# Optimization experiments

Measured on AMD Instinct MI355X. Metric: run time of the kernel, lower is better.

## Reference

```python
import jax, jax.numpy as jnp
import numpy as np

L, H, D, DFF, B, S = 4, 8, 512, 2048, 2, 2048
DH = D // H
EPS = 1e-5
SCALE_BASE = 512.0


def setup_inputs() -> dict:
    key = jax.random.key(0)
    ks = jax.random.split(key, 8)
    def w(k, shape, s=0.02):
        return jax.random.normal(k, shape, jnp.float32) * s
    return {
        "x": jax.random.normal(ks[0], (B, S, D), jnp.float32),
        "WQ": w(ks[1], (L, H, D, DH)),
        "WK": w(ks[2], (L, H, D, DH)),
        "WV": w(ks[3], (L, H, D, DH)),
        "WG": w(ks[4], (L, D, D)),
        "WO": w(ks[5], (L, D, D)),
        "gn_w": jnp.ones((L, D), jnp.float32),
        "gn_b": jnp.zeros((L, D), jnp.float32),
        "ln1_w": jnp.ones((L, D), jnp.float32),
        "ln1_b": jnp.zeros((L, D), jnp.float32),
        "ln2_w": jnp.ones((L, D), jnp.float32),
        "ln2_b": jnp.zeros((L, D), jnp.float32),
        "ffn_w1": w(ks[6], (L, D, DFF)),
        "ffn_b1": jnp.zeros((L, DFF), jnp.float32),
        "ffn_w2": w(ks[7], (L, DFF, D)),
        "ffn_b2": jnp.zeros((L, D), jnp.float32),
    }


def _dup(t):
    # duplicate_interleave: [a,b] -> [a,a,b,b]
    return jnp.repeat(t, 2, axis=-1)


def _rot(x):
    # rotate_every_two: (x1,x2) -> (-x2, x1)
    x1, x2 = x[..., ::2], x[..., 1::2]
    return jnp.stack([-x2, x1], axis=-1).reshape(x.shape)


def _xpos(x, downscale):
    # x: [B,H,S,dh]  XPOS rotary with length-extrapolating scale
    s_len, dh = x.shape[-2], x.shape[-1]
    half = dh // 2
    base = (jnp.arange(0, dh, 2, dtype=jnp.float32) + 0.4 * dh) / (1.4 * dh)  # [half]
    power = jnp.arange(s_len, dtype=jnp.float32) / SCALE_BASE
    scale = base[None, :] ** power[:, None]  # [S, half]
    if downscale:
        scale = 1.0 / scale
    inv_freq = 1.0 / (10000.0 ** (jnp.arange(half, dtype=jnp.float32) / half))
    ang = jnp.arange(s_len, dtype=jnp.float32)[:, None] * inv_freq[None, :]
    sin, cos, sc = _dup(jnp.sin(ang)), _dup(jnp.cos(ang)), _dup(scale)
    return x * cos * sc + _rot(x) * sin * sc


def _ln(x, w, b):
    mu = jnp.mean(x, -1, keepdims=True)
    var = jnp.mean((x - mu) ** 2, -1, keepdims=True)
    return (x - mu) * jax.lax.rsqrt(var + EPS) * w + b


def reference(x, WQ, WK, WV, WG, WO, gn_w, gn_b, ln1_w, ln1_b, ln2_w, ln2_b, ffn_w1, ffn_b1, ffn_w2, ffn_b2):
    gammas = 1.0 - jnp.exp(jnp.linspace(np.log(1.0 / 32.0), np.log(1.0 / 512.0), H)).astype(jnp.float32)
    idx = jnp.arange(S, dtype=jnp.float32)
    diff = idx[:, None] - idx[None, :]
    Dmask = jnp.where(diff >= 0, gammas[:, None, None] ** diff, 0.0)  # [H,S,S]
    b = x.shape[0]
    for i in range(L):
        xn = _ln(x, ln1_w[i], ln1_b[i])
        q = _xpos(jnp.einsum('bsd,hde->bhse', xn, WQ[i]), False)
        k = _xpos(jnp.einsum('bsd,hde->bhse', xn, WK[i]), True)
        v = jnp.einsum('bsd,hde->bhse', xn, WV[i])
        att = jnp.einsum('bhse,bhte->bhst', q, k) * Dmask[None]  # [B,H,S,S]
        yh = jnp.einsum('bhst,bhte->bhse', att, v)               # [B,H,S,dh]
        yh = yh.transpose(0, 2, 1, 3)                            # [B,S,H,dh]
        mu = jnp.mean(yh, -1, keepdims=True)
        var = jnp.mean((yh - mu) ** 2, -1, keepdims=True)
        yn = (yh - mu) * jax.lax.rsqrt(var + EPS)
        yn = yn * gn_w[i].reshape(H, DH) + gn_b[i].reshape(H, DH)
        y = yn.reshape(b, S, D)
        g = jax.nn.silu(xn @ WG[i])
        y1 = (g * y) @ WO[i] + x
        h = _ln(y1, ln2_w[i], ln2_b[i])
        x = jax.nn.gelu(h @ ffn_w1[i] + ffn_b1[i], approximate=False) @ ffn_w2[i] + ffn_b2[i] + y1
    return x
```

## Files before the change

kernel.cpp:

```cpp
#include <hip/hip_runtime.h>
#include <hip/hip_bf16.h>

#define LYR 4
#define NH  8
#define DM  512
#define DHD 64
#define DFF 2048
#define BB  2
#define SSL 2048
#define NROWS (BB*SSL)

typedef unsigned short u16;
typedef __attribute__((ext_vector_type(8))) short bf16x8;
typedef __attribute__((ext_vector_type(4))) float f32x4;
typedef __attribute__((ext_vector_type(4))) unsigned int u32x4;

__device__ __forceinline__ u16 f2bf(float f) {
    union { float f; unsigned u; } v; v.f = f;
    unsigned r = v.u + 0x7FFFu + ((v.u >> 16) & 1u);
    return (u16)(r >> 16);
}
__device__ __forceinline__ float bf2f(u16 b) {
    union { unsigned u; float f; } v; v.u = ((unsigned)b) << 16;
    return v.f;
}
__device__ __forceinline__ int swz(int row, int col) {
    return row * 64 + (col & 7) + ((((col >> 3) ^ row) & 7) << 3);
}
__device__ __forceinline__ void gload16(const u16* g, u16* l) {
    __builtin_amdgcn_global_load_lds(
        (const __attribute__((address_space(1))) unsigned int*)g,
        (__attribute__((address_space(3))) unsigned int*)l, 16, 0, 0);
}
template <int N> __device__ __forceinline__ void wait_vmcnt() {
    if constexpr (N == 0)      asm volatile("s_waitcnt vmcnt(0)" ::: "memory");
    else if constexpr (N == 6) asm volatile("s_waitcnt vmcnt(6)" ::: "memory");
    else static_assert(N == 0 || N == 6, "unsupported vmcnt");
}
__device__ __forceinline__ void block_barrier() {
    __builtin_amdgcn_s_barrier();
    asm volatile("" ::: "memory");
}


__global__ __launch_bounds__(256) void xpos_tables(float4* __restrict__ tab4) {
    const int idx = blockIdx.x * 256 + threadIdx.x;
    const int s = idx >> 5, j = idx & 31;
    const float base = (2.f * j + 0.4f * 64.f) / (1.4f * 64.f);
    const float invf = powf(10000.f, -(float)j / 32.f);
    const float ang = (float)s * invf;
    const float scq = powf(base, (float)s / 512.f);
    tab4[idx] = make_float4(sinf(ang), cosf(ang), scq, 1.f / scq);
}

__global__ __launch_bounds__(256)
void prep_qkv(const float* __restrict__ WQp, const float* __restrict__ WKp,
              const float* __restrict__ WVp, u16* __restrict__ WBT) {
    const int dt = blockIdx.x;
    const int h = blockIdx.y & 7, which = blockIdx.y >> 3;
    const int l = blockIdx.z;
    const float* W = (which == 0 ? WQp : which == 1 ? WKp : WVp);
    const float* ip = W + ((size_t)(l * 8 + h)) * (512 * 64);
    u16* op = WBT + (size_t)l * (2048 * 512) + (size_t)(which * 512 + h * 64) * 512;
    __shared__ u16 tile[64 * 72];
    const int t = threadIdx.x, rr = t >> 2, cc = (t & 3) * 16;
    const float* src = ip + (size_t)(dt * 64 + rr) * 64 + cc;
#pragma unroll
    for (int i = 0; i < 16; ++i) tile[rr * 72 + cc + i] = f2bf(src[i]);
    __syncthreads();
    u16 tmp[16] __attribute__((aligned(16)));
#pragma unroll
    for (int i = 0; i < 16; ++i) tmp[i] = tile[(cc + i) * 72 + rr];
    u16* dst = op + (size_t)rr * 512 + dt * 64 + cc;
    *(u32x4*)&dst[0] = *(const u32x4*)&tmp[0];
    *(u32x4*)&dst[8] = *(const u32x4*)&tmp[8];
}

__global__ __launch_bounds__(256)
void prep_t(const float* __restrict__ in, u16* __restrict__ out, int R, int C,
            long long in_ls, long long out_ls) {
    const float* ip = in + (size_t)blockIdx.z * in_ls;
    u16* op = out + (size_t)blockIdx.z * out_ls;
    const int r0 = blockIdx.x * 64, c0t = blockIdx.y * 64;
    __shared__ u16 tile[64 * 72];
    const int t = threadIdx.x, rr = t >> 2, cc = (t & 3) * 16;
    const float* src = ip + (size_t)(r0 + rr) * C + c0t + cc;
#pragma unroll
    for (int i = 0; i < 16; ++i) tile[rr * 72 + cc + i] = f2bf(src[i]);
    __syncthreads();
    u16 tmp[16] __attribute__((aligned(16)));
#pragma unroll
    for (int i = 0; i < 16; ++i) tmp[i] = tile[(cc + i) * 72 + rr];
    u16* dst = op + (size_t)(c0t + rr) * R + r0 + cc;
    *(u32x4*)&dst[0] = *(const u32x4*)&tmp[0];
    *(u32x4*)&dst[8] = *(const u32x4*)&tmp[8];
}

__global__ __launch_bounds__(256)
void ln_kernel(const float* __restrict__ x, const float* __restrict__ wt,
               const float* __restrict__ bs, u16* __restrict__ out) {
    const int row = blockIdx.x * 4 + (threadIdx.x >> 6);
    const int lane = threadIdx.x & 63;
    const float* xr = x + (size_t)row * DM + lane * 8;
    float v[8];
    *(float4*)&v[0] = *(const float4*)&xr[0];
    *(float4*)&v[4] = *(const float4*)&xr[4];
    float s = 0.f, s2 = 0.f;
#pragma unroll
    for (int i = 0; i < 8; ++i) { s += v[i]; s2 += v[i] * v[i]; }
#pragma unroll
    for (int m = 1; m < 64; m <<= 1) {
        s  += __shfl_xor(s, m, 64);
        s2 += __shfl_xor(s2, m, 64);
    }
    const float mu = s * (1.f / DM);
    const float rs = rsqrtf(s2 * (1.f / DM) - mu * mu + 1e-5f);
    const int e0 = lane * 8;
    u16 o[8] __attribute__((aligned(16)));
#pragma unroll
    for (int i = 0; i < 8; ++i)
        o[i] = f2bf((v[i] - mu) * rs * wt[e0 + i] + bs[e0 + i]);
    *(u32x4*)&out[(size_t)row * DM + e0] = *(const u32x4*)o;
}

template <int BM, int BN, int EPI>
__global__ __launch_bounds__(256)
void gemm_bt(const u16* __restrict__ A, const u16* __restrict__ Bt,
             u16* __restrict__ obf, float* __restrict__ of32,
             const float* __restrict__ res, const float* __restrict__ bias,
             int M, int N, int K) {
    constexpr int FM = BM / 32, FN = BN / 32;
    constexpr int LPS = BM / 32 + BN / 32;
    static_assert(LPS == 6, "vmcnt template expects 6");
    __shared__ __align__(16) u16 As[2][BM * 64];
    __shared__ __align__(16) u16 Bs[2][BN * 64];
    const int t = threadIdx.x;
    const int lane = t & 63, w4 = t >> 6;
    const int wr = w4 >> 1, wc = w4 & 1;
    const int fr = lane & 15, fq = lane >> 4;
    const int nX = N / BN;
    const int nwg = (M / BM) * nX;
    const int swzid = (blockIdx.x & 7) * (nwg >> 3) + (blockIdx.x >> 3);
    const int m0 = (swzid / nX) * BM, n0 = (swzid % nX) * BN;
    const int lr = lane >> 3;
    const int ls = lane & 7;
    const int nsteps = K >> 6;

    auto stage = [&](int step, int slot) {
        const int k0 = step << 6;
#pragma unroll
        for (int q = 0; q < BM / 32; ++q) {
            const int ib = q * 4 + w4;
            const int row = ib * 8 + lr;
            const int cc = ls ^ (row & 7);
            gload16(&A[(size_t)(m0 + row) * K + k0 + cc * 8], &As[slot][ib * 512]);
        }
#pragma unroll
        for (int q = 0; q < BN / 32; ++q) {
            const int ib = q * 4 + w4;
            const int row = ib * 8 + lr;
            const int cc = ls ^ (row & 7);
            gload16(&Bt[(size_t)(n0 + row) * K + k0 + cc * 8], &Bs[slot][ib * 512]);
        }
    };

    f32x4 acc[FM][FN] = {};
    stage(0, 0);
    stage(1, 1);
    for (int st = 0; st < nsteps; ++st) {
        if (st + 1 < nsteps) wait_vmcnt<LPS>(); else wait_vmcnt<0>();
        __builtin_amdgcn_sched_barrier(0);
        block_barrier();
        const u16* Ac = As[st & 1];
        const u16* Bc = Bs[st & 1];
#pragma unroll
        for (int ks = 0; ks < 2; ++ks) {
            bf16x8 av[FM], bv[FN];
#pragma unroll
            for (int i = 0; i < FM; ++i)
                av[i] = *(const bf16x8*)&Ac[swz(wr * (BM / 2) + i * 16 + fr, ks * 32 + fq * 8)];
#pragma unroll
            for (int j = 0; j < FN; ++j)
                bv[j] = *(const bf16x8*)&Bc[swz(wc * (BN / 2) + j * 16 + fr, ks * 32 + fq * 8)];
#pragma unroll
            for (int i = 0; i < FM; ++i)
#pragma unroll
                for (int j = 0; j < FN; ++j)
                    acc[i][j] = __builtin_amdgcn_mfma_f32_16x16x32_bf16(av[i], bv[j], acc[i][j], 0, 0, 0);
        }
        asm volatile("s_waitcnt lgkmcnt(0)" ::: "memory");
        __builtin_amdgcn_sched_barrier(0);
        block_barrier();
        if (st + 2 < nsteps) stage(st + 2, st & 1);
    }
#pragma unroll
    for (int i = 0; i < FM; ++i)
#pragma unroll
        for (int j = 0; j < FN; ++j)
#pragma unroll
            for (int r = 0; r < 4; ++r) {
                const int m = m0 + wr * (BM / 2) + i * 16 + fq * 4 + r;
                const int n = n0 + wc * (BN / 2) + j * 16 + fr;
                const size_t idx = (size_t)m * N + n;
                float v = acc[i][j][r];
                if constexpr (EPI == 1) {
                    of32[idx] = v + res[idx];
                } else {
                    of32[idx] = v + bias[n] + res[idx];
                }
            }
}

template <int EPI>
__global__ __launch_bounds__(512, 1)
void gemm_big(const u16* __restrict__ A, const u16* __restrict__ Bt,
              u16* __restrict__ obf, const float* __restrict__ bias,
              u16* __restrict__ qb, u16* __restrict__ kb, u16* __restrict__ kt,
              u16* __restrict__ vt, u16* __restrict__ gb,
              const float4* __restrict__ tab4, int M, int N, int K) {
    constexpr int BM = 256, BN = 128;
    __shared__ __align__(16) u16 SM[49152];
    const int t = threadIdx.x;
    const int lane = t & 63, w = t >> 6;
    const int wr4 = w >> 1, wc2 = w & 1;
    const int fr = lane & 15, fq = lane >> 4;
    const int nX = N / BN;
    const int nwg = (M / BM) * nX;
    const int swzid = (blockIdx.x & 7) * (nwg >> 3) + (blockIdx.x >> 3);
    const int m0 = (swzid / nX) * BM, n0 = (swzid % nX) * BN;
    const int lr = lane >> 3, ls = lane & 7;
    const int nsteps = K >> 6;

    auto stage = [&](int step, int slot) {
        const int k0 = step << 6;
#pragma unroll
        for (int q = 0; q < 4; ++q) {
            const int ib = q * 8 + w;
            const int row = ib * 8 + lr;
            const int cc = ls ^ (row & 7);
            gload16(&A[(size_t)(m0 + row) * K + k0 + cc * 8], &SM[slot * 16384 + ib * 512]);
        }
#pragma unroll
        for (int q = 0; q < 2; ++q) {
            const int ib = q * 8 + w;
            const int row = ib * 8 + lr;
            const int cc = ls ^ (row & 7);
            gload16(&Bt[(size_t)(n0 + row) * K + k0 + cc * 8],
                    &SM[32768 + slot * 8192 + ib * 512]);
        }
    };

    f32x4 acc[4][4] = {};
    stage(0, 0);
    stage(1, 1);
    for (int st = 0; st < nsteps; ++st) {
        if (st + 1 < nsteps) wait_vmcnt<6>(); else wait_vmcnt<0>();
        __builtin_amdgcn_sched_barrier(0);
        block_barrier();
        const u16* Ac = &SM[(st & 1) * 16384];
        const u16* Bc = &SM[32768 + (st & 1) * 8192];
#pragma unroll
        for (int ks = 0; ks < 2; ++ks) {
            bf16x8 av[4], bv[4];
#pragma unroll
            for (int i = 0; i < 4; ++i)
                av[i] = *(const bf16x8*)&Ac[swz(wr4 * 64 + i * 16 + fr, ks * 32 + fq * 8)];
#pragma unroll
            for (int j = 0; j < 4; ++j)
                bv[j] = *(const bf16x8*)&Bc[swz(wc2 * 64 + j * 16 + fr, ks * 32 + fq * 8)];
            __builtin_amdgcn_s_setprio(1);
#pragma unroll
            for (int i = 0; i < 4; ++i)
#pragma unroll
                for (int j = 0; j < 4; ++j)
                    acc[i][j] = __builtin_amdgcn_mfma_f32_16x16x32_bf16(av[i], bv[j], acc[i][j], 0, 0, 0);
            __builtin_amdgcn_s_setprio(0);
        }
        asm volatile("s_waitcnt lgkmcnt(0)" ::: "memory");
        __builtin_amdgcn_sched_barrier(0);
        block_barrier();
        if (st + 2 < nsteps) stage(st + 2, st & 1);
    }

    if constexpr (EPI == 2) {
#pragma unroll
        for (int i = 0; i < 4; ++i)
#pragma unroll
            for (int j = 0; j < 4; ++j)
#pragma unroll
                for (int r = 0; r < 4; ++r) {
                    const int m = m0 + wr4 * 64 + i * 16 + fq * 4 + r;
                    const int n = n0 + wc2 * 64 + j * 16 + fr;
                    float tt = acc[i][j][r] + bias[n];
                    obf[(size_t)m * N + n] = f2bf(0.5f * tt * (1.f + erff(tt * 0.7071067811865475f)));
                }
    } else {
        const int region = n0 >> 9;
        const int h = (n0 & 511) >> 6;
        const int b = m0 >> 11;
        const int s0 = m0 & 2047;
        if (region == 3) {
#pragma unroll
            for (int i = 0; i < 4; ++i)
#pragma unroll
                for (int j = 0; j < 4; ++j)
#pragma unroll
                    for (int r = 0; r < 4; ++r) {
                        const int m = m0 + wr4 * 64 + i * 16 + fq * 4 + r;
                        const int el = wc2 * 64 + j * 16 + fr;
                        gb[(size_t)m * 512 + (n0 & 511) + el] = f2bf(acc[i][j][r]);
                    }
        } else if (region <= 1) {
            u16* dst = (region == 0) ? qb : kb;
            u16* LT = SM;
#pragma unroll
            for (int i = 0; i < 4; ++i)
#pragma unroll
                for (int j = 0; j < 4; ++j)
#pragma unroll
                    for (int r = 0; r < 4; ++r) {
                        const int sl = wr4 * 64 + i * 16 + fq * 4 + r;
                        const int s = s0 + sl;
                        const int el = wc2 * 64 + j * 16 + fr;
                        const int hh = h + (el >> 6), e = el & 63;
                        const float v = acc[i][j][r];
                        const float p = __shfl_xor(v, 1, 64);
                        const float rot = (e & 1) ? p : -p;
                        const float4 t4 = tab4[(size_t)s * 32 + (e >> 1)];
                        const float scl = (region == 0) ? t4.z : t4.w;
                        const u16 bv = f2bf((v * t4.y + rot * t4.x) * scl);
                        dst[((size_t)(b * NH + hh) * 2048 + s) * 64 + e] = bv;
                        if (region == 1) LT[el * 264 + sl] = bv;
                    }
            if (region == 1) {
                __syncthreads();
                for (int c = t; c < 128 * 32; c += 512) {
                    const int er = c >> 5;
                    const int sc = (c & 31) * 8;
                    const int hh = h + (er >> 6), e = er & 63;
                    *(u32x4*)&kt[((size_t)(b * NH + hh) * 64 + e) * 2048 + s0 + sc] =
                        *(const u32x4*)&LT[er * 264 + sc];
                }
            }
        } else {
            u16* LT = SM;
#pragma unroll
            for (int i = 0; i < 4; ++i)
#pragma unroll
                for (int j = 0; j < 4; ++j)
#pragma unroll
                    for (int r = 0; r < 4; ++r) {
                        const int sl = wr4 * 64 + i * 16 + fq * 4 + r;
                        const int el = wc2 * 64 + j * 16 + fr;
                        LT[el * 264 + sl] = f2bf(acc[i][j][r]);
                    }
            __syncthreads();
            for (int c = t; c < 128 * 32; c += 512) {
                const int er = c >> 5;
                const int sc = (c & 31) * 8;
                const int hh = h + (er >> 6), e = er & 63;
                *(u32x4*)&vt[((size_t)(b * NH + hh) * 64 + e) * 2048 + s0 + sc] =
                    *(const u32x4*)&LT[er * 264 + sc];
            }
        }
    }
}

__global__ __launch_bounds__(512)
void ret_intra(const u16* __restrict__ Qb, const u16* __restrict__ Kb,
               const u16* __restrict__ Kt, const u16* __restrict__ Vt,
               float* __restrict__ OI, float* __restrict__ Tb) {
    __shared__ __align__(16) u16 Ks[64 * 64];
    __shared__ __align__(16) u16 KTs[64 * 64];
    __shared__ __align__(16) u16 Vs[64 * 64];
    __shared__ __align__(16) u16 Ps[64 * 64];
    const int logical = (blockIdx.x & 7) * 64 + (blockIdx.x >> 3);
    const int bh = logical >> 5, n = logical & 31;
    const int h = bh & 7;
    const int t = threadIdx.x, lane = t & 63, w = t >> 6;
    const int fr = lane & 15, fq = lane >> 4;
    const int wr = w & 1, wc = w >> 1;
    const float gamma = 1.f - expf(-3.4657359f + (float)h * -0.39608410f);
    const float lgam = log2f(gamma);
    const size_t bh2048 = (size_t)bh * 2048;
    {
        const int r8 = lane >> 3, g8 = lane & 7;
        const int row = w * 8 + r8;
        const int cc = g8 ^ (row & 7);
        gload16(&Kb[(bh2048 + n * 64 + row) * 64 + cc * 8], &Ks[w * 512]);
        gload16(&Kt[((size_t)bh * 64 + row) * 2048 + n * 64 + cc * 8], &KTs[w * 512]);
        gload16(&Vt[((size_t)bh * 64 + row) * 2048 + n * 64 + cc * 8], &Vs[w * 512]);
    }
    bf16x8 qa[2][2];
#pragma unroll
    for (int i = 0; i < 2; ++i)
#pragma unroll
        for (int ks = 0; ks < 2; ++ks)
            qa[i][ks] = *(const bf16x8*)&Qb[(bh2048 + n * 64 + wr * 32 + i * 16 + fr) * 64
                                           + ks * 32 + fq * 8];
    asm volatile("s_waitcnt vmcnt(0)" ::: "memory");
    block_barrier();
    f32x4 sac[2] = {};
#pragma unroll
    for (int ks = 0; ks < 2; ++ks) {
        bf16x8 kv = *(const bf16x8*)&Ks[swz(wc * 16 + fr, ks * 32 + fq * 8)];
#pragma unroll
        for (int i = 0; i < 2; ++i)
            sac[i] = __builtin_amdgcn_mfma_f32_16x16x32_bf16(qa[i][ks], kv, sac[i], 0, 0, 0);
    }
#pragma unroll
    for (int i = 0; i < 2; ++i)
#pragma unroll
        for (int rr = 0; rr < 4; ++rr) {
            const int row = wr * 32 + i * 16 + fq * 4 + rr;
            const int col = wc * 16 + fr;
            const int d = row - col;
            const float mval = (d >= 0) ? exp2f(lgam * (float)d) : 0.f;
            Ps[swz(row, col)] = f2bf(sac[i][rr] * mval);
        }
    __syncthreads();
    f32x4 oacc[2] = {}, tacc[2] = {};
    const float gi = exp2f(-lgam);
#pragma unroll
    for (int ks = 0; ks < 2; ++ks) {
        bf16x8 vb = *(const bf16x8*)&Vs[swz(wc * 16 + fr, ks * 32 + fq * 8)];
        bf16x8 ktb = *(const bf16x8*)&KTs[swz(wc * 16 + fr, ks * 32 + fq * 8)];
#pragma unroll
        for (int i = 0; i < 2; ++i) {
            bf16x8 pa = *(const bf16x8*)&Ps[swz(wr * 32 + i * 16 + fr, ks * 32 + fq * 8)];
            oacc[i] = __builtin_amdgcn_mfma_f32_16x16x32_bf16(pa, vb, oacc[i], 0, 0, 0);
            bf16x8 vv = *(const bf16x8*)&Vs[swz(wr * 32 + i * 16 + fr, ks * 32 + fq * 8)];
            bf16x8 vw;
            float wgt = exp2f(lgam * (float)(64 - ks * 32 - fq * 8));
#pragma unroll
            for (int j = 0; j < 8; ++j) {
                vw[j] = (short)f2bf(bf2f((u16)vv[j]) * wgt);
                wgt *= gi;
            }
            tacc[i] = __builtin_amdgcn_mfma_f32_16x16x32_bf16(vw, ktb, tacc[i], 0, 0, 0);
        }
    }
#pragma unroll
    for (int i = 0; i < 2; ++i)
#pragma unroll
        for (int rr = 0; rr < 4; ++rr) {
            const int row = wr * 32 + i * 16 + fq * 4 + rr;
            const int col = wc * 16 + fr;
            OI[(bh2048 + n * 64 + row) * 64 + col] = oacc[i][rr];
            Tb[((size_t)(bh * 32 + n)) * 4096 + row * 64 + col] = tacc[i][rr];
        }
}

__global__ __launch_bounds__(512)
void ret_inter(const u16* __restrict__ Qb, const float* __restrict__ Tb,
               const float* __restrict__ OI, const u16* __restrict__ gate,
               const float* __restrict__ gnw, const float* __restrict__ gnb,
               u16* __restrict__ zb) {
    __shared__ __align__(16) u16 Ss[64 * 64];
    __shared__ float Of[64 * 66];
    const int logical = (blockIdx.x & 7) * 64 + (blockIdx.x >> 3);
    const int bh = logical >> 5, n = logical & 31;
    const int h = bh & 7, b = bh >> 3;
    const int t = threadIdx.x, lane = t & 63, w = t >> 6;
    const int fr = lane & 15, fq = lane >> 4;
    const float gamma = 1.f - expf(-3.4657359f + (float)h * -0.39608410f);
    const float lgam = log2f(gamma);
    const size_t bh2048 = (size_t)bh * 2048;
    {
        const int ev = t >> 3, ek0 = (t & 7) * 8;
        float sacc[8] = {0.f, 0.f, 0.f, 0.f, 0.f, 0.f, 0.f, 0.f};
        for (int m = n - 1; m >= 0; --m) {
            const float wgt = exp2f(lgam * 64.f * (float)(n - 1 - m));
            if (wgt < 1e-12f) break;
            const float* src = &Tb[((size_t)(bh * 32 + m)) * 4096 + ev * 64 + ek0];
#pragma unroll
            for (int j = 0; j < 8; ++j) sacc[j] += wgt * src[j];
        }
#pragma unroll
        for (int j = 0; j < 8; ++j) Ss[swz(ev, ek0 + j)] = f2bf(sacc[j]);
    }
    __syncthreads();
    f32x4 oacc[2] = {};
    const int iq = w & 3, j2 = w >> 2;
    if (n > 0) {
        const float qs = exp2f(lgam * (float)(iq * 16 + fr));
#pragma unroll
        for (int ks = 0; ks < 2; ++ks) {
            bf16x8 qv = *(const bf16x8*)&Qb[(bh2048 + n * 64 + iq * 16 + fr) * 64
                                           + ks * 32 + fq * 8];
            bf16x8 qw;
#pragma unroll
            for (int j = 0; j < 8; ++j) qw[j] = (short)f2bf(bf2f((u16)qv[j]) * qs);
#pragma unroll
            for (int jj = 0; jj < 2; ++jj) {
                bf16x8 sv = *(const bf16x8*)&Ss[swz(j2 * 32 + jj * 16 + fr, ks * 32 + fq * 8)];
                oacc[jj] = __builtin_amdgcn_mfma_f32_16x16x32_bf16(qw, sv, oacc[jj], 0, 0, 0);
            }
        }
    }
#pragma unroll
    for (int jj = 0; jj < 2; ++jj)
#pragma unroll
        for (int r = 0; r < 4; ++r)
            Of[(iq * 16 + fq * 4 + r) * 66 + j2 * 32 + jj * 16 + fr] = oacc[jj][r];
    __syncthreads();
    const int row = t >> 3, c0 = (t & 7) * 8;
    float v[8];
    float s = 0.f, s2 = 0.f;
    const float* oi = &OI[(bh2048 + n * 64 + row) * 64 + c0];
#pragma unroll
    for (int i = 0; i < 8; ++i) {
        v[i] = Of[row * 66 + c0 + i] + oi[i];
        s += v[i]; s2 += v[i] * v[i];
    }
    s  += __shfl_xor(s, 1, 64);  s  += __shfl_xor(s, 2, 64);  s  += __shfl_xor(s, 4, 64);
    s2 += __shfl_xor(s2, 1, 64); s2 += __shfl_xor(s2, 2, 64); s2 += __shfl_xor(s2, 4, 64);
    const float mu = s * (1.f / 64.f);
    const float rs = rsqrtf(s2 * (1.f / 64.f) - mu * mu + 1e-5f);
    const int sg = n * 64 + row;
    u16 gv[8] __attribute__((aligned(16)));
    *(u32x4*)gv = *(const u32x4*)&gate[((size_t)(b * SSL + sg)) * 512 + h * 64 + c0];
    u16 ob[8] __attribute__((aligned(16)));
#pragma unroll
    for (int i = 0; i < 8; ++i) {
        const int dc = h * 64 + c0 + i;
        const float yn = (v[i] - mu) * rs * gnw[dc] + gnb[dc];
        const float g = bf2f(gv[i]);
        ob[i] = f2bf(yn * (g / (1.f + expf(-g))));
    }
    *(u32x4*)&zb[((size_t)(b * SSL + sg)) * 512 + h * 64 + c0] = *(const u32x4*)ob;
}

extern "C" void kernel_launch(void* const* d_in, const int* in_sizes, int n_in,
                              void* d_out, int out_size, void* d_ws, size_t ws_size,
                              hipStream_t stream) {
    const float* X    = (const float*)d_in[0];
    const float* WQ   = (const float*)d_in[1];
    const float* WK   = (const float*)d_in[2];
    const float* WV   = (const float*)d_in[3];
    const float* WG   = (const float*)d_in[4];
    const float* WO   = (const float*)d_in[5];
    const float* GNW  = (const float*)d_in[6];
    const float* GNB  = (const float*)d_in[7];
    const float* LN1W = (const float*)d_in[8];
    const float* LN1B = (const float*)d_in[9];
    const float* LN2W = (const float*)d_in[10];
    const float* LN2B = (const float*)d_in[11];
    const float* FW1  = (const float*)d_in[12];
    const float* FB1  = (const float*)d_in[13];
    const float* FW2  = (const float*)d_in[14];
    const float* FB2  = (const float*)d_in[15];

    char* ws = (char*)d_ws;
    size_t off = 0;
    auto alloc = [&](size_t n) { char* p = ws + off; off += (n + 255) & ~(size_t)255; return p; };

    u16*   WBT  = (u16*)alloc((size_t)LYR * 2048 * 512 * 2);
    u16*   WOT  = (u16*)alloc((size_t)LYR * 512 * 512 * 2);
    u16*   W1T  = (u16*)alloc((size_t)LYR * 2048 * 512 * 2);
    u16*   W2T  = (u16*)alloc((size_t)LYR * 512 * 2048 * 2);
    float4* TAB4 = (float4*)alloc((size_t)2048 * 32 * 16);
    float* XB   = (float*)alloc((size_t)NROWS * DM * 4);
    u16*   XN   = (u16*)alloc((size_t)NROWS * DM * 2);
    u16*   FF1  = (u16*)alloc((size_t)NROWS * 2048 * 2);
    u16*   GB   = (u16*)alloc((size_t)NROWS * DM * 2);
    u16*   QBp  = (u16*)alloc((size_t)NROWS * DM * 2);
    u16*   KBp  = (u16*)alloc((size_t)NROWS * DM * 2);
    u16*   KTp  = (u16*)alloc((size_t)NROWS * DM * 2);
    u16*   VTp  = (u16*)alloc((size_t)NROWS * DM * 2);
    u16*   ZB   = (u16*)alloc((size_t)NROWS * DM * 2);
    float* Y1   = (float*)alloc((size_t)NROWS * DM * 4);
    u16*   HB   = QBp;
    float* Tb   = (float*)FF1;
    float* OIb  = (float*)(FF1 + 4194304);

    xpos_tables<<<256, 256, 0, stream>>>(TAB4);
    prep_qkv<<<dim3(8, 24, LYR), 256, 0, stream>>>(WQ, WK, WV, WBT);
    prep_t<<<dim3(8, 8, LYR), 256, 0, stream>>>(WG, WBT + 1536 * 512, 512, 512,
                                                (long long)512 * 512, (long long)2048 * 512);
    prep_t<<<dim3(8, 8, LYR), 256, 0, stream>>>(WO, WOT, 512, 512,
                                                (long long)512 * 512, (long long)512 * 512);
    prep_t<<<dim3(8, 32, LYR), 256, 0, stream>>>(FW1, W1T, 512, 2048,
                                                 (long long)512 * 2048, (long long)2048 * 512);
    prep_t<<<dim3(32, 8, LYR), 256, 0, stream>>>(FW2, W2T, 2048, 512,
                                                 (long long)2048 * 512, (long long)512 * 2048);

    for (int l = 0; l < LYR; ++l) {
        const float* xsrc = (l == 0) ? X : XB;
        float* xdst = (l == LYR - 1) ? (float*)d_out : XB;
        ln_kernel<<<NROWS / 4, 256, 0, stream>>>(xsrc, LN1W + l * 512, LN1B + l * 512, XN);
        gemm_big<4><<<256, 512, 0, stream>>>(
            XN, WBT + (size_t)l * 2048 * 512, nullptr, nullptr,
            QBp, KBp, KTp, VTp, GB, TAB4, NROWS, 2048, 512);
        ret_intra<<<512, 512, 0, stream>>>(QBp, KBp, KTp, VTp, OIb, Tb);
        ret_inter<<<512, 512, 0, stream>>>(QBp, Tb, OIb, GB,
                                           GNW + l * 512, GNB + l * 512, ZB);
        gemm_bt<64, 128, 1><<<256, 256, 0, stream>>>(
            ZB, WOT + (size_t)l * 512 * 512, nullptr, Y1, xsrc, nullptr, NROWS, 512, 512);
        ln_kernel<<<NROWS / 4, 256, 0, stream>>>(Y1, LN2W + l * 512, LN2B + l * 512, HB);
        gemm_big<2><<<256, 512, 0, stream>>>(
            HB, W1T + (size_t)l * 2048 * 512, FF1, FB1 + l * 2048,
            nullptr, nullptr, nullptr, nullptr, nullptr, nullptr, NROWS, 2048, 512);
        gemm_bt<64, 128, 3><<<256, 256, 0, stream>>>(
            FF1, W2T + (size_t)l * 512 * 2048, nullptr, xdst, Y1, FB2 + l * 512, NROWS, 512, 2048);
    }
}
```

Measured before the change: 482.0 us.

## Split retention into chunk-state kernel and fused intra+inter main kernel

The intra-chunk attention (QK^T masked, PV) moves out of the first kernel and into the second, which now also handles the inter-chunk state contribution. The float intra-chunk output no longer round-trips through global memory. The per-chunk state T is now stored as bf16 with coalesced 16-byte writes, and the decayed prefix sum uses an incremental weight with a precomputed loop bound. This cuts global traffic between the two retention kernels, at the cost of extra bf16 rounding in the state sum and more LDS and work in the second kernel.

Result: faster. 470.0 us (-2.5%).

```diff
diff --git a/kernel.cpp b/kernel.cpp
--- a/kernel.cpp
+++ b/kernel.cpp
@@ -367,13 +367,11 @@
 }
 
 __global__ __launch_bounds__(512)
-void ret_intra(const u16* __restrict__ Qb, const u16* __restrict__ Kb,
-               const u16* __restrict__ Kt, const u16* __restrict__ Vt,
-               float* __restrict__ OI, float* __restrict__ Tb) {
-    __shared__ __align__(16) u16 Ks[64 * 64];
+void ret_tchunk(const u16* __restrict__ Kt, const u16* __restrict__ Vt,
+                u16* __restrict__ Tb) {
     __shared__ __align__(16) u16 KTs[64 * 64];
     __shared__ __align__(16) u16 Vs[64 * 64];
-    __shared__ __align__(16) u16 Ps[64 * 64];
+    __shared__ __align__(16) u16 Ts[64 * 64];
     const int logical = (blockIdx.x & 7) * 64 + (blockIdx.x >> 3);
     const int bh = logical >> 5, n = logical & 31;
     const int h = bh & 7;
@@ -382,53 +380,22 @@
     const int wr = w & 1, wc = w >> 1;
     const float gamma = 1.f - expf(-3.4657359f + (float)h * -0.39608410f);
     const float lgam = log2f(gamma);
-    const size_t bh2048 = (size_t)bh * 2048;
     {
-        const int r8 = lane >> 3, g8 = lane & 7;
-        const int row = w * 8 + r8;
+        const int r8_ = lane >> 3, g8 = lane & 7;
+        const int row = w * 8 + r8_;
         const int cc = g8 ^ (row & 7);
-        gload16(&Kb[(bh2048 + n * 64 + row) * 64 + cc * 8], &Ks[w * 512]);
         gload16(&Kt[((size_t)bh * 64 + row) * 2048 + n * 64 + cc * 8], &KTs[w * 512]);
         gload16(&Vt[((size_t)bh * 64 + row) * 2048 + n * 64 + cc * 8], &Vs[w * 512]);
     }
-    bf16x8 qa[2][2];
-#pragma unroll
-    for (int i = 0; i < 2; ++i)
-#pragma unroll
-        for (int ks = 0; ks < 2; ++ks)
-            qa[i][ks] = *(const bf16x8*)&Qb[(bh2048 + n * 64 + wr * 32 + i * 16 + fr) * 64
-                                           + ks * 32 + fq * 8];
     asm volatile("s_waitcnt vmcnt(0)" ::: "memory");
     block_barrier();
-    f32x4 sac[2] = {};
+    f32x4 tacc[2] = {};
+    const float gi = exp2f(-lgam);
 #pragma unroll
     for (int ks = 0; ks < 2; ++ks) {
-        bf16x8 kv = *(const bf16x8*)&Ks[swz(wc * 16 + fr, ks * 32 + fq * 8)];
-#pragma unroll
-        for (int i = 0; i < 2; ++i)
-            sac[i] = __builtin_amdgcn_mfma_f32_16x16x32_bf16(qa[i][ks], kv, sac[i], 0, 0, 0);
-    }
-#pragma unroll
-    for (int i = 0; i < 2; ++i)
-#pragma unroll
-        for (int rr = 0; rr < 4; ++rr) {
-            const int row = wr * 32 + i * 16 + fq * 4 + rr;
-            const int col = wc * 16 + fr;
-            const int d = row - col;
-            const float mval = (d >= 0) ? exp2f(lgam * (float)d) : 0.f;
-            Ps[swz(row, col)] = f2bf(sac[i][rr] * mval);
-        }
-    __syncthreads();
-    f32x4 oacc[2] = {}, tacc[2] = {};
-    const float gi = exp2f(-lgam);
-#pragma unroll
-    for (int ks = 0; ks < 2; ++ks) {
-        bf16x8 vb = *(const bf16x8*)&Vs[swz(wc * 16 + fr, ks * 32 + fq * 8)];
         bf16x8 ktb = *(const bf16x8*)&KTs[swz(wc * 16 + fr, ks * 32 + fq * 8)];
 #pragma unroll
         for (int i = 0; i < 2; ++i) {
-            bf16x8 pa = *(const bf16x8*)&Ps[swz(wr * 32 + i * 16 + fr, ks * 32 + fq * 8)];
-            oacc[i] = __builtin_amdgcn_mfma_f32_16x16x32_bf16(pa, vb, oacc[i], 0, 0, 0);
             bf16x8 vv = *(const bf16x8*)&Vs[swz(wr * 32 + i * 16 + fr, ks * 32 + fq * 8)];
             bf16x8 vw;
             float wgt = exp2f(lgam * (float)(64 - ks * 32 - fq * 8));
@@ -443,19 +410,20 @@
 #pragma unroll
     for (int i = 0; i < 2; ++i)
 #pragma unroll
-        for (int rr = 0; rr < 4; ++rr) {
-            const int row = wr * 32 + i * 16 + fq * 4 + rr;
-            const int col = wc * 16 + fr;
-            OI[(bh2048 + n * 64 + row) * 64 + col] = oacc[i][rr];
-            Tb[((size_t)(bh * 32 + n)) * 4096 + row * 64 + col] = tacc[i][rr];
-        }
+        for (int rr = 0; rr < 4; ++rr)
+            Ts[(wr * 32 + i * 16 + fq * 4 + rr) * 64 + wc * 16 + fr] = f2bf(tacc[i][rr]);
+    __syncthreads();
+    *(u32x4*)&Tb[((size_t)(bh * 32 + n)) * 4096 + t * 8] = *(const u32x4*)&Ts[t * 8];
 }
 
 __global__ __launch_bounds__(512)
-void ret_inter(const u16* __restrict__ Qb, const float* __restrict__ Tb,
-               const float* __restrict__ OI, const u16* __restrict__ gate,
-               const float* __restrict__ gnw, const float* __restrict__ gnb,
-               u16* __restrict__ zb) {
+void ret_main(const u16* __restrict__ Qb, const u16* __restrict__ Kb,
+              const u16* __restrict__ Vt, const u16* __restrict__ Tb,
+              const u16* __restrict__ gate, const float* __restrict__ gnw,
+              const float* __restrict__ gnb, u16* __restrict__ zb) {
+    __shared__ __align__(16) u16 Ks[64 * 64];
+    __shared__ __align__(16) u16 Vs[64 * 64];
+    __shared__ __align__(16) u16 Ps[64 * 64];
     __shared__ __align__(16) u16 Ss[64 * 64];
     __shared__ float Of[64 * 66];
     const int logical = (blockIdx.x & 7) * 64 + (blockIdx.x >> 3);
@@ -463,38 +431,94 @@
     const int h = bh & 7, b = bh >> 3;
     const int t = threadIdx.x, lane = t & 63, w = t >> 6;
     const int fr = lane & 15, fq = lane >> 4;
+    const int wr = w & 1, wc = w >> 1;
+    const int iq = w & 3, j2 = w >> 2;
     const float gamma = 1.f - expf(-3.4657359f + (float)h * -0.39608410f);
     const float lgam = log2f(gamma);
     const size_t bh2048 = (size_t)bh * 2048;
     {
-        const int ev = t >> 3, ek0 = (t & 7) * 8;
-        float sacc[8] = {0.f, 0.f, 0.f, 0.f, 0.f, 0.f, 0.f, 0.f};
-        for (int m = n - 1; m >= 0; --m) {
-            const float wgt = exp2f(lgam * 64.f * (float)(n - 1 - m));
-            if (wgt < 1e-12f) break;
-            const float* src = &Tb[((size_t)(bh * 32 + m)) * 4096 + ev * 64 + ek0];
-#pragma unroll
-            for (int j = 0; j < 8; ++j) sacc[j] += wgt * src[j];
-        }
-#pragma unroll
-        for (int j = 0; j < 8; ++j) Ss[swz(ev, ek0 + j)] = f2bf(sacc[j]);
-    }
+        const int r8_ = lane >> 3, g8 = lane & 7;
+        const int row = w * 8 + r8_;
+        const int cc = g8 ^ (row & 7);
+        gload16(&Kb[(bh2048 + n * 64 + row) * 64 + cc * 8], &Ks[w * 512]);
+        gload16(&Vt[((size_t)bh * 64 + row) * 2048 + n * 64 + cc * 8], &Vs[w * 512]);
+    }
+    bf16x8 qi[2][2], qe[2];
+#pragma unroll
+    for (int ks = 0; ks < 2; ++ks) {
+#pragma unroll
+        for (int i = 0; i < 2; ++i)
+            qi[i][ks] = *(const bf16x8*)&Qb[(bh2048 + n * 64 + wr * 32 + i * 16 + fr) * 64
+                                           + ks * 32 + fq * 8];
+        qe[ks] = *(const bf16x8*)&Qb[(bh2048 + n * 64 + iq * 16 + fr) * 64 + ks * 32 + fq * 8];
+    }
+    float sacc[8] = {0.f, 0.f, 0.f, 0.f, 0.f, 0.f, 0.f, 0.f};
+    if (n > 0) {
+        const int span = (int)(19.931568f / (-lgam * 64.f));
+        int m_min = n - 1 - span;
+        if (m_min < 0) m_min = 0;
+        float wgt = 1.f;
+        const float g64 = exp2f(64.f * lgam);
+        const u16* base = &Tb[(size_t)bh * 32 * 4096 + t * 8];
+        for (int m = n - 1; m >= m_min; --m) {
+            const u32x4 raw = *(const u32x4*)&base[(size_t)m * 4096];
+#pragma unroll
+            for (int j = 0; j < 4; ++j) {
+                const unsigned u = raw[j];
+                sacc[2 * j]     += wgt * bf2f((u16)(u & 0xffff));
+                sacc[2 * j + 1] += wgt * bf2f((u16)(u >> 16));
+            }
+            wgt *= g64;
+        }
+    }
+    {
+        u16 tmp[8] __attribute__((aligned(16)));
+#pragma unroll
+        for (int j = 0; j < 8; ++j) tmp[j] = f2bf(sacc[j]);
+        *(u32x4*)&Ss[swz(t >> 3, (t & 7) * 8)] = *(const u32x4*)tmp;
+    }
+    asm volatile("s_waitcnt vmcnt(0)" ::: "memory");
     __syncthreads();
-    f32x4 oacc[2] = {};
-    const int iq = w & 3, j2 = w >> 2;
+    f32x4 sac[2] = {};
+#pragma unroll
+    for (int ks = 0; ks < 2; ++ks) {
+        bf16x8 kv = *(const bf16x8*)&Ks[swz(wc * 16 + fr, ks * 32 + fq * 8)];
+#pragma unroll
+        for (int i = 0; i < 2; ++i)
+            sac[i] = __builtin_amdgcn_mfma_f32_16x16x32_bf16(qi[i][ks], kv, sac[i], 0, 0, 0);
+    }
+#pragma unroll
+    for (int i = 0; i < 2; ++i)
+#pragma unroll
+        for (int rr = 0; rr < 4; ++rr) {
+            const int row = wr * 32 + i * 16 + fq * 4 + rr;
+            const int col = wc * 16 + fr;
+            const int d = row - col;
+            const float mval = (d >= 0) ? exp2f(lgam * (float)d) : 0.f;
+            Ps[swz(row, col)] = f2bf(sac[i][rr] * mval);
+        }
+    __syncthreads();
+    f32x4 opv[2] = {}, oqs[2] = {};
+#pragma unroll
+    for (int ks = 0; ks < 2; ++ks) {
+        bf16x8 vb = *(const bf16x8*)&Vs[swz(wc * 16 + fr, ks * 32 + fq * 8)];
+#pragma unroll
+        for (int i = 0; i < 2; ++i) {
+            bf16x8 pa = *(const bf16x8*)&Ps[swz(wr * 32 + i * 16 + fr, ks * 32 + fq * 8)];
+            opv[i] = __builtin_amdgcn_mfma_f32_16x16x32_bf16(pa, vb, opv[i], 0, 0, 0);
+        }
+    }
     if (n > 0) {
         const float qs = exp2f(lgam * (float)(iq * 16 + fr));
 #pragma unroll
         for (int ks = 0; ks < 2; ++ks) {
-            bf16x8 qv = *(const bf16x8*)&Qb[(bh2048 + n * 64 + iq * 16 + fr) * 64
-                                           + ks * 32 + fq * 8];
             bf16x8 qw;
 #pragma unroll
-            for (int j = 0; j < 8; ++j) qw[j] = (short)f2bf(bf2f((u16)qv[j]) * qs);
+            for (int j = 0; j < 8; ++j) qw[j] = (short)f2bf(bf2f((u16)qe[ks][j]) * qs);
 #pragma unroll
             for (int jj = 0; jj < 2; ++jj) {
                 bf16x8 sv = *(const bf16x8*)&Ss[swz(j2 * 32 + jj * 16 + fr, ks * 32 + fq * 8)];
-                oacc[jj] = __builtin_amdgcn_mfma_f32_16x16x32_bf16(qw, sv, oacc[jj], 0, 0, 0);
+                oqs[jj] = __builtin_amdgcn_mfma_f32_16x16x32_bf16(qw, sv, oqs[jj], 0, 0, 0);
             }
         }
     }
@@ -502,15 +526,20 @@
     for (int jj = 0; jj < 2; ++jj)
 #pragma unroll
         for (int r = 0; r < 4; ++r)
-            Of[(iq * 16 + fq * 4 + r) * 66 + j2 * 32 + jj * 16 + fr] = oacc[jj][r];
+            Of[(iq * 16 + fq * 4 + r) * 66 + j2 * 32 + jj * 16 + fr] = oqs[jj][r];
+    __syncthreads();
+#pragma unroll
+    for (int i = 0; i < 2; ++i)
+#pragma unroll
+        for (int rr = 0; rr < 4; ++rr)
+            Of[(wr * 32 + i * 16 + fq * 4 + rr) * 66 + wc * 16 + fr] += opv[i][rr];
     __syncthreads();
     const int row = t >> 3, c0 = (t & 7) * 8;
     float v[8];
     float s = 0.f, s2 = 0.f;
-    const float* oi = &OI[(bh2048 + n * 64 + row) * 64 + c0];
 #pragma unroll
     for (int i = 0; i < 8; ++i) {
-        v[i] = Of[row * 66 + c0 + i] + oi[i];
+        v[i] = Of[row * 66 + c0 + i];
         s += v[i]; s2 += v[i] * v[i];
     }
     s  += __shfl_xor(s, 1, 64);  s  += __shfl_xor(s, 2, 64);  s  += __shfl_xor(s, 4, 64);
@@ -571,8 +600,7 @@
     u16*   ZB   = (u16*)alloc((size_t)NROWS * DM * 2);
     float* Y1   = (float*)alloc((size_t)NROWS * DM * 4);
     u16*   HB   = QBp;
-    float* Tb   = (float*)FF1;
-    float* OIb  = (float*)(FF1 + 4194304);
+    u16*   Tb   = FF1;
 
     xpos_tables<<<256, 256, 0, stream>>>(TAB4);
     prep_qkv<<<dim3(8, 24, LYR), 256, 0, stream>>>(WQ, WK, WV, WBT);
@@ -592,9 +620,9 @@
         gemm_big<4><<<256, 512, 0, stream>>>(
             XN, WBT + (size_t)l * 2048 * 512, nullptr, nullptr,
             QBp, KBp, KTp, VTp, GB, TAB4, NROWS, 2048, 512);
-        ret_intra<<<512, 512, 0, stream>>>(QBp, KBp, KTp, VTp, OIb, Tb);
-        ret_inter<<<512, 512, 0, stream>>>(QBp, Tb, OIb, GB,
-                                           GNW + l * 512, GNB + l * 512, ZB);
+        ret_tchunk<<<512, 512, 0, stream>>>(KTp, VTp, Tb);
+        ret_main<<<512, 512, 0, stream>>>(QBp, KBp, VTp, Tb, GB,
+                                          GNW + l * 512, GNB + l * 512, ZB);
         gemm_bt<64, 128, 1><<<256, 256, 0, stream>>>(
             ZB, WOT + (size_t)l * 512 * 512, nullptr, Y1, xsrc, nullptr, NROWS, 512, 512);
         ln_kernel<<<NROWS / 4, 256, 0, stream>>>(Y1, LN2W + l * 512, LN2B + l * 512, HB);
```
